# Kernel tuning notes

Hardware: AMD Instinct MI355X
Metric: run time of the kernel (lower is better)

The kernel has to match this reference:

```python
import jax, jax.numpy as jnp
import numpy as np
from jax import lax

B, T = 2, 2048
D = 512        # d_model
K = 64         # k_lookback (causal window)


def setup_inputs() -> dict:
    key = jax.random.key(0)
    k1, k2, k3 = jax.random.split(key, 3)
    x = jax.random.normal(k1, (B, 1, T), jnp.float32)
    conv_w = jax.random.normal(k2, (D, 1, 3), jnp.float32) * 0.2
    conv_b = jax.random.normal(k3, (D,), jnp.float32) * 0.05
    gate = jnp.array(0.5, jnp.float32)  # nn.Parameter scalar
    return {"x": x, "conv_w": conv_w, "conv_b": conv_b, "gate": gate}


def reference(x, conv_w, conv_b, gate):
    # feature_proj: Conv1d(1, D, k=3, pad=1) + exact GELU (dropout inactive at eval)
    q = lax.conv_general_dilated(
        x, conv_w, window_strides=(1,), padding=[(1, 1)],
        dimension_numbers=("NCH", "OIH", "NCH"))
    q = jax.nn.gelu(q + conv_b[None, :, None], approximate=False)  # [B, D, T]

    # causal sliding windows: keys_windows[b,c,t,j] = q[b,c, t-(K-1)+j] (0 outside)
    padded = jnp.pad(q, ((0, 0), (0, 0), (K - 1, 0)))
    idx = jnp.arange(T)[:, None] + jnp.arange(K)[None, :]  # [T, K]
    kw = padded[:, :, idx]                                  # [B, D, T, K]

    energy = jnp.einsum("bct,bctk->btk", q, kw)             # [B, T, K]
    attn = jax.nn.softmax(energy / np.float32(np.sqrt(D)), axis=-1)
    context = jnp.einsum("btk,bctk->bct", attn, kw)         # [B, D, T]
    return context * jnp.tanh(gate)
```

## Files before the change

### kernel.cpp

```cpp
#include <hip/hip_runtime.h>
#include <math.h>

#define B 2
#define T 2048
#define D 512
#define KW 64
#define SCALE 0.044194173824159216f

#define RQ (64 + T + 16)
#define TTP (64 + T + 16)

typedef __attribute__((ext_vector_type(8))) short short8;
typedef __attribute__((ext_vector_type(4))) float f32x4;

__device__ __forceinline__ ushort f2bf(float f) {
  union { float f; unsigned u; } v; v.f = f;
  unsigned r = v.u + 0x7fffu + ((v.u >> 16) & 1u);
  return (ushort)(r >> 16);
}

__device__ __forceinline__ float gelu_fast(float v) {
  float v2 = v * v;
  float u  = fmaf(v2 * v, 0.03567740814f, 0.7978845608f * v);
  float e  = __builtin_amdgcn_exp2f(2.885390082f * u);
  float r  = __builtin_amdgcn_rcpf(1.f + e);
  return fmaf(-v, r, v);
}

__global__ __launch_bounds__(256) void k_conv(
    const float* __restrict__ x, const float* __restrict__ w,
    const float* __restrict__ bias, ushort* __restrict__ q,
    ushort* __restrict__ qT) {
  int blk = blockIdx.x;
  int tid = threadIdx.x;

  if (blk >= 512) {
    int ztid = (blk - 512) * 256 + tid;
    const uint4 z = {0u, 0u, 0u, 0u};
    for (int task = ztid; task < 20480; task += 2048) {
      size_t e;
      if (task < 8192) {
        int b = task >> 12, i = task & 4095;
        e = (size_t)b * RQ * D + (size_t)i * 8;
      } else if (task < 10240) {
        int idx = task - 8192;
        int b = idx >> 10, i = idx & 1023;
        e = (size_t)b * RQ * D + (size_t)(64 + T) * D + (size_t)i * 8;
      } else if (task < 18432) {
        int idx = task - 10240;
        int r = idx >> 3, i = idx & 7;
        e = (size_t)r * TTP + (size_t)i * 8;
        *(uint4*)(qT + e) = z;
        continue;
      } else {
        int idx = task - 18432;
        int r = idx >> 1, i = idx & 1;
        e = (size_t)r * TTP + 64 + T + (size_t)i * 8;
        *(uint4*)(qT + e) = z;
        continue;
      }
      *(uint4*)(q + e) = z;
    }
    return;
  }

  __shared__ float s_tile[64 * 65];

  int xcd = blk & 7;
  int i   = blk >> 3;
  int b   = xcd >> 2;
  int t0  = (xcd & 3) * 512 + (i >> 3) * 64;
  int c0  = (i & 7) * 64;

  int lt = tid >> 2;
  int cb = (tid & 3) << 4;
  int t = t0 + lt;
  float xm1 = (t > 0)     ? x[b * T + t - 1] : 0.f;
  float x0  =               x[b * T + t];
  float xp1 = (t < T - 1) ? x[b * T + t + 1] : 0.f;

  float wf[48], bf[16];
#pragma unroll
  for (int v4 = 0; v4 < 12; ++v4)
    *(float4*)&wf[v4 * 4] = *(const float4*)(w + (size_t)(c0 + cb) * 3 + v4 * 4);
#pragma unroll
  for (int v4 = 0; v4 < 4; ++v4)
    *(float4*)&bf[v4 * 4] = *(const float4*)(bias + c0 + cb + v4 * 4);

  short8 h0, h1;
#pragma unroll
  for (int e = 0; e < 16; ++e) {
    float v = fmaf(xm1, wf[e * 3], fmaf(x0, wf[e * 3 + 1],
              fmaf(xp1, wf[e * 3 + 2], bf[e])));
    float g = gelu_fast(v);
    s_tile[lt * 65 + cb + e] = g;
    if (e < 8) h0[e] = (short)f2bf(g); else h1[e - 8] = (short)f2bf(g);
  }
  {
    ushort* qp = q + ((size_t)b * RQ + 64 + t) * D + c0 + cb;
    *(short8*)qp = h0;
    *(short8*)(qp + 8) = h1;
  }
  __syncthreads();

  int lc = tid >> 2;
  int tb = (tid & 3) << 4;
  short8 v0, v1;
#pragma unroll
  for (int e = 0; e < 8; ++e)
    v0[e] = (short)f2bf(s_tile[(tb + e) * 65 + lc]);
#pragma unroll
  for (int e = 0; e < 8; ++e)
    v1[e] = (short)f2bf(s_tile[(tb + 8 + e) * 65 + lc]);
  {
    ushort* qp = qT + ((size_t)b * D + c0 + lc) * TTP + 64 + t0 + tb;
    *(short8*)qp = v0;
    *(short8*)(qp + 8) = v1;
  }
}

__global__ __launch_bounds__(256, 1) void k_attn(
    const ushort* __restrict__ q, const ushort* __restrict__ qT,
    const float* __restrict__ gate, float* __restrict__ out) {
  __shared__ alignas(16) f32x4 s_E[4 * 5 * 64];
  __shared__ alignas(16) ushort s_attn[4][16 * 96];

  int blk  = blockIdx.x;
  int tile = (blk & 7) * 32 + (blk >> 3);
  int b  = tile >> 7;
  int t0 = (tile & 127) << 4;
  int tid  = threadIdx.x;
  int wv   = tid >> 6;
  int lane = tid & 63;
  int n    = lane & 15;
  int quad = lane >> 4;

  const ushort* qb = q + (size_t)b * RQ * D + (size_t)64 * D;
  const ushort* qTb = qT + (size_t)b * D * TTP;

  short8 afr[4], bfr[4][5];
#pragma unroll
  for (int i = 0; i < 4; ++i) {
    int cofs = (wv * 4 + i) * 32 + quad * 8;
    afr[i] = *(const short8*)(qb + (size_t)(t0 + n) * D + cofs);
#pragma unroll
    for (int jc = 0; jc < 5; ++jc) {
      int tp = t0 - (KW - 1) + jc * 16 + n;
      bfr[i][jc] = *(const short8*)(qb + (ptrdiff_t)tp * D + cofs);
    }
  }
  short8 bfr2[8][3];
#pragma unroll
  for (int ncl = 0; ncl < 8; ++ncl) {
    int c = (wv * 8 + ncl) * 16 + n;
#pragma unroll
    for (int ks = 0; ks < 3; ++ks)
      bfr2[ncl][ks] =
          *(const short8*)(qTb + (size_t)c * TTP + t0 + ks * 32 + quad * 8);
  }

  f32x4 acc[5];
#pragma unroll
  for (int jc = 0; jc < 5; ++jc) acc[jc] = (f32x4){0.f, 0.f, 0.f, 0.f};
#pragma unroll
  for (int i = 0; i < 4; ++i)
#pragma unroll
    for (int jc = 0; jc < 5; ++jc)
      acc[jc] = __builtin_amdgcn_mfma_f32_16x16x32_bf16(afr[i], bfr[i][jc],
                                                        acc[jc], 0, 0, 0);

#pragma unroll
  for (int jc = 0; jc < 5; ++jc)
    s_E[(wv * 5 + jc) * 64 + lane] = acc[jc];
  __syncthreads();

#pragma unroll
  for (int ww = 0; ww < 4; ++ww) {
    if (ww == wv) continue;
#pragma unroll
    for (int jc = 0; jc < 5; ++jc) {
      f32x4 v = s_E[(ww * 5 + jc) * 64 + lane];
      acc[jc][0] += v[0]; acc[jc][1] += v[1];
      acc[jc][2] += v[2]; acc[jc][3] += v[3];
    }
  }

  ushort* sa = s_attn[wv];
#pragma unroll
  for (int r = 0; r < 4; ++r) {
    int m = quad * 4 + r;
    float e[5];
    float mx = -1e30f;
#pragma unroll
    for (int jc = 0; jc < 5; ++jc) {
      int j = jc * 16 + n;
      bool valid = (j >= m) && (j <= m + (KW - 1));
      e[jc] = valid ? acc[jc][r] * SCALE : -1e30f;
      mx = fmaxf(mx, e[jc]);
    }
#pragma unroll
    for (int off = 1; off <= 8; off <<= 1) mx = fmaxf(mx, __shfl_xor(mx, off, 64));
    float p[5];
    float s = 0.f;
#pragma unroll
    for (int jc = 0; jc < 5; ++jc) {
      p[jc] = (e[jc] > -1e29f) ? __expf(e[jc] - mx) : 0.f;
      s += p[jc];
    }
#pragma unroll
    for (int off = 1; off <= 8; off <<= 1) s += __shfl_xor(s, off, 64);
    float inv = 1.f / s;
#pragma unroll
    for (int jc = 0; jc < 5; ++jc) {
      int j = jc * 16 + n;
      sa[m * 96 + j + 1] = f2bf(p[jc] * inv);
    }
    int jp = (n == 0) ? 0 : (80 + n);
    sa[m * 96 + jp] = 0;
  }

  short8 afr2[3];
#pragma unroll
  for (int ks = 0; ks < 3; ++ks)
    afr2[ks] = *(const short8*)(sa + n * 96 + ks * 32 + quad * 8);

  const float tg = tanhf(gate[0]);
#pragma unroll
  for (int ncl = 0; ncl < 8; ++ncl) {
    int c = (wv * 8 + ncl) * 16 + n;
    f32x4 co = (f32x4){0.f, 0.f, 0.f, 0.f};
#pragma unroll
    for (int ks = 0; ks < 3; ++ks)
      co = __builtin_amdgcn_mfma_f32_16x16x32_bf16(afr2[ks], bfr2[ncl][ks],
                                                   co, 0, 0, 0);
    f32x4 o;
    o[0] = co[0] * tg; o[1] = co[1] * tg; o[2] = co[2] * tg; o[3] = co[3] * tg;
    *(f32x4*)(out + ((size_t)b * D + c) * T + t0 + quad * 4) = o;
  }
}

extern "C" void kernel_launch(void* const* d_in, const int* in_sizes, int n_in,
                              void* d_out, int out_size, void* d_ws, size_t ws_size,
                              hipStream_t stream) {
  const float* x      = (const float*)d_in[0];
  const float* conv_w = (const float*)d_in[1];
  const float* conv_b = (const float*)d_in[2];
  const float* gate   = (const float*)d_in[3];
  float* out = (float*)d_out;

  ushort* q_ws  = (ushort*)d_ws;
  ushort* qT_ws = q_ws + (size_t)B * RQ * D;

  k_conv<<<520, 256, 0, stream>>>(x, conv_w, conv_b, q_ws, qT_ws);
  k_attn<<<B * T / 16, 256, 0, stream>>>(q_ws, qT_ws, gate, out);
}
```

Measured before the change: 76.27 us.

## Fuse conv+GELU into attention kernel, recompute q window in LDS

Removes the separate conv kernel and its global q/qT workspace. Each attention block now recomputes the conv+GELU features for its 96-row causal window directly into swizzled shared memory, then transposes them in place for the second MFMA. This drops a kernel launch and the global bf16 round-trip, including the workspace zeroing. The cost is redundant recomputation (about 6x per row), 96KB of LDS per block, and extra barriers for the in-LDS transpose.

```diff
diff --git a/kernel.cpp b/kernel.cpp
--- a/kernel.cpp
+++ b/kernel.cpp
@@ -6,9 +6,6 @@
 #define D 512
 #define KW 64
 #define SCALE 0.044194173824159216f
-
-#define RQ (64 + T + 16)
-#define TTP (64 + T + 16)
 
 typedef __attribute__((ext_vector_type(8))) short short8;
 typedef __attribute__((ext_vector_type(4))) float f32x4;
@@ -27,136 +24,66 @@
   return fmaf(-v, r, v);
 }
 
-__global__ __launch_bounds__(256) void k_conv(
+__device__ __forceinline__ int qt_off(int j, int c) {
+  return j * 512 + (c ^ ((j & 7) << 3));
+}
+__device__ __forceinline__ int qc_off(int c, int j) {
+  return (j >> 5) * 16384 + c * 32 + ((j & 31) ^ (((c >> 1) & 3) << 3));
+}
+
+__global__ __launch_bounds__(256, 1) void k_fused(
     const float* __restrict__ x, const float* __restrict__ w,
-    const float* __restrict__ bias, ushort* __restrict__ q,
-    ushort* __restrict__ qT) {
-  int blk = blockIdx.x;
-  int tid = threadIdx.x;
-
-  if (blk >= 512) {
-    int ztid = (blk - 512) * 256 + tid;
-    const uint4 z = {0u, 0u, 0u, 0u};
-    for (int task = ztid; task < 20480; task += 2048) {
-      size_t e;
-      if (task < 8192) {
-        int b = task >> 12, i = task & 4095;
-        e = (size_t)b * RQ * D + (size_t)i * 8;
-      } else if (task < 10240) {
-        int idx = task - 8192;
-        int b = idx >> 10, i = idx & 1023;
-        e = (size_t)b * RQ * D + (size_t)(64 + T) * D + (size_t)i * 8;
-      } else if (task < 18432) {
-        int idx = task - 10240;
-        int r = idx >> 3, i = idx & 7;
-        e = (size_t)r * TTP + (size_t)i * 8;
-        *(uint4*)(qT + e) = z;
-        continue;
-      } else {
-        int idx = task - 18432;
-        int r = idx >> 1, i = idx & 1;
-        e = (size_t)r * TTP + 64 + T + (size_t)i * 8;
-        *(uint4*)(qT + e) = z;
-        continue;
-      }
-      *(uint4*)(q + e) = z;
-    }
-    return;
-  }
-
-  __shared__ float s_tile[64 * 65];
-
-  int xcd = blk & 7;
-  int i   = blk >> 3;
-  int b   = xcd >> 2;
-  int t0  = (xcd & 3) * 512 + (i >> 3) * 64;
-  int c0  = (i & 7) * 64;
-
-  int lt = tid >> 2;
-  int cb = (tid & 3) << 4;
-  int t = t0 + lt;
-  float xm1 = (t > 0)     ? x[b * T + t - 1] : 0.f;
-  float x0  =               x[b * T + t];
-  float xp1 = (t < T - 1) ? x[b * T + t + 1] : 0.f;
-
-  float wf[48], bf[16];
-#pragma unroll
-  for (int v4 = 0; v4 < 12; ++v4)
-    *(float4*)&wf[v4 * 4] = *(const float4*)(w + (size_t)(c0 + cb) * 3 + v4 * 4);
-#pragma unroll
-  for (int v4 = 0; v4 < 4; ++v4)
-    *(float4*)&bf[v4 * 4] = *(const float4*)(bias + c0 + cb + v4 * 4);
-
-  short8 h0, h1;
-#pragma unroll
-  for (int e = 0; e < 16; ++e) {
-    float v = fmaf(xm1, wf[e * 3], fmaf(x0, wf[e * 3 + 1],
-              fmaf(xp1, wf[e * 3 + 2], bf[e])));
-    float g = gelu_fast(v);
-    s_tile[lt * 65 + cb + e] = g;
-    if (e < 8) h0[e] = (short)f2bf(g); else h1[e - 8] = (short)f2bf(g);
-  }
-  {
-    ushort* qp = q + ((size_t)b * RQ + 64 + t) * D + c0 + cb;
-    *(short8*)qp = h0;
-    *(short8*)(qp + 8) = h1;
-  }
-  __syncthreads();
-
-  int lc = tid >> 2;
-  int tb = (tid & 3) << 4;
-  short8 v0, v1;
-#pragma unroll
-  for (int e = 0; e < 8; ++e)
-    v0[e] = (short)f2bf(s_tile[(tb + e) * 65 + lc]);
-#pragma unroll
-  for (int e = 0; e < 8; ++e)
-    v1[e] = (short)f2bf(s_tile[(tb + 8 + e) * 65 + lc]);
-  {
-    ushort* qp = qT + ((size_t)b * D + c0 + lc) * TTP + 64 + t0 + tb;
-    *(short8*)qp = v0;
-    *(short8*)(qp + 8) = v1;
-  }
-}
-
-__global__ __launch_bounds__(256, 1) void k_attn(
-    const ushort* __restrict__ q, const ushort* __restrict__ qT,
-    const float* __restrict__ gate, float* __restrict__ out) {
+    const float* __restrict__ bias, const float* __restrict__ gate,
+    float* __restrict__ out) {
+  __shared__ alignas(16) ushort s_q[96 * 512];
   __shared__ alignas(16) f32x4 s_E[4 * 5 * 64];
-  __shared__ alignas(16) ushort s_attn[4][16 * 96];
+  __shared__ ushort s_attn[4][16 * 96];
 
   int blk  = blockIdx.x;
-  int tile = (blk & 7) * 32 + (blk >> 3);
-  int b  = tile >> 7;
-  int t0 = (tile & 127) << 4;
+  int b    = blk >> 7;
+  int t0   = (blk & 127) << 4;
   int tid  = threadIdx.x;
   int wv   = tid >> 6;
   int lane = tid & 63;
   int n    = lane & 15;
   int quad = lane >> 4;
 
-  const ushort* qb = q + (size_t)b * RQ * D + (size_t)64 * D;
-  const ushort* qTb = qT + (size_t)b * D * TTP;
+  int c0 = lane * 8;
+  float wf[24], bf[8];
+#pragma unroll
+  for (int v4 = 0; v4 < 6; ++v4)
+    *(float4*)&wf[v4 * 4] = *(const float4*)(w + (size_t)c0 * 3 + v4 * 4);
+#pragma unroll
+  for (int v4 = 0; v4 < 2; ++v4)
+    *(float4*)&bf[v4 * 4] = *(const float4*)(bias + c0 + v4 * 4);
+  const float* xb = x + (size_t)b * T;
+
+  for (int it = 0; it < 24; ++it) {
+    int j  = wv + it * 4;
+    int tp = t0 - 64 + j;
+    bool inr = (unsigned)tp < (unsigned)T;
+    float xm1 = ((unsigned)(tp - 1) < (unsigned)T) ? xb[tp - 1] : 0.f;
+    float x0  = inr                    ? xb[tp]     : 0.f;
+    float xp1 = ((unsigned)(tp + 1) < (unsigned)T) ? xb[tp + 1] : 0.f;
+    short8 pk;
+#pragma unroll
+    for (int e = 0; e < 8; ++e) {
+      float v = fmaf(xm1, wf[e * 3], fmaf(x0, wf[e * 3 + 1],
+                fmaf(xp1, wf[e * 3 + 2], bf[e])));
+      pk[e] = inr ? (short)f2bf(gelu_fast(v)) : (short)0;
+    }
+    *(short8*)&s_q[qt_off(j, c0)] = pk;
+  }
+  __syncthreads();
 
   short8 afr[4], bfr[4][5];
 #pragma unroll
   for (int i = 0; i < 4; ++i) {
     int cofs = (wv * 4 + i) * 32 + quad * 8;
-    afr[i] = *(const short8*)(qb + (size_t)(t0 + n) * D + cofs);
-#pragma unroll
-    for (int jc = 0; jc < 5; ++jc) {
-      int tp = t0 - (KW - 1) + jc * 16 + n;
-      bfr[i][jc] = *(const short8*)(qb + (ptrdiff_t)tp * D + cofs);
-    }
-  }
-  short8 bfr2[8][3];
-#pragma unroll
-  for (int ncl = 0; ncl < 8; ++ncl) {
-    int c = (wv * 8 + ncl) * 16 + n;
-#pragma unroll
-    for (int ks = 0; ks < 3; ++ks)
-      bfr2[ncl][ks] =
-          *(const short8*)(qTb + (size_t)c * TTP + t0 + ks * 32 + quad * 8);
+    afr[i] = *(const short8*)&s_q[qt_off(64 + n, cofs)];
+#pragma unroll
+    for (int jc = 0; jc < 5; ++jc)
+      bfr[i][jc] = *(const short8*)&s_q[qt_off(1 + jc * 16 + n, cofs)];
   }
 
   f32x4 acc[5];
@@ -218,11 +145,30 @@
     int jp = (n == 0) ? 0 : (80 + n);
     sa[m * 96 + jp] = 0;
   }
-
   short8 afr2[3];
 #pragma unroll
   for (int ks = 0; ks < 3; ++ks)
     afr2[ks] = *(const short8*)(sa + n * 96 + ks * 32 + quad * 8);
+
+  for (int k = 0; k < 3; ++k) {
+    short8 tr[8];
+#pragma unroll
+    for (int g = 0; g < 8; ++g) {
+      int c  = tid + ((g & 1) << 8);
+      int j0 = (g >> 1) << 3;
+#pragma unroll
+      for (int e = 0; e < 8; ++e)
+        tr[g][e] = (short)s_q[qt_off(k * 32 + j0 + e, c)];
+    }
+    __syncthreads();
+#pragma unroll
+    for (int g = 0; g < 8; ++g) {
+      int c  = tid + ((g & 1) << 8);
+      int j0 = (g >> 1) << 3;
+      *(short8*)&s_q[qc_off(c, k * 32 + j0)] = tr[g];
+    }
+    __syncthreads();
+  }
 
   const float tg = tanhf(gate[0]);
 #pragma unroll
@@ -230,9 +176,10 @@
     int c = (wv * 8 + ncl) * 16 + n;
     f32x4 co = (f32x4){0.f, 0.f, 0.f, 0.f};
 #pragma unroll
-    for (int ks = 0; ks < 3; ++ks)
-      co = __builtin_amdgcn_mfma_f32_16x16x32_bf16(afr2[ks], bfr2[ncl][ks],
-                                                   co, 0, 0, 0);
+    for (int ks = 0; ks < 3; ++ks) {
+      short8 bfr2 = *(const short8*)&s_q[qc_off(c, ks * 32 + quad * 8)];
+      co = __builtin_amdgcn_mfma_f32_16x16x32_bf16(afr2[ks], bfr2, co, 0, 0, 0);
+    }
     f32x4 o;
     o[0] = co[0] * tg; o[1] = co[1] * tg; o[2] = co[2] * tg; o[3] = co[3] * tg;
     *(f32x4*)(out + ((size_t)b * D + c) * T + t0 + quad * 4) = o;
@@ -247,10 +194,7 @@
   const float* conv_b = (const float*)d_in[2];
   const float* gate   = (const float*)d_in[3];
   float* out = (float*)d_out;
-
-  ushort* q_ws  = (ushort*)d_ws;
-  ushort* qT_ws = q_ws + (size_t)B * RQ * D;
-
-  k_conv<<<520, 256, 0, stream>>>(x, conv_w, conv_b, q_ws, qT_ws);
-  k_attn<<<B * T / 16, 256, 0, stream>>>(q_ws, qT_ws, gate, out);
-}
+  (void)d_ws; (void)ws_size;
+
+  k_fused<<<B * T / 16, 256, 0, stream>>>(x, conv_w, conv_b, gate, out);
+}
```

Result: slower. 82.16 us (+7.7%).
